# Kernel optimization log

Hardware: AMD Instinct MI355X
Metric: run time of the kernel (lower is better)

Reference implementation:

```python
import jax, jax.numpy as jnp
import numpy as np

GAMMA = 0.99
RHO_THRESHOLD = 1.0
C_THRESHOLD = 1.0
BASELINE_LOSS_SCALING = 0.5
ENT_COEFF = 0.01
PPO_CLIP = 0.2


def setup_inputs() -> dict:
    key = jax.random.key(0)
    ks = jax.random.split(key, 7)
    T, B, A = 512, 8192, 2
    return {
        "prob": jax.random.uniform(ks[0], (T, B, A), dtype=jnp.float32),
        "action_prob": jax.random.uniform(ks[1], (T, B, A), dtype=jnp.float32),
        "v": jax.random.normal(ks[2], (T, B), dtype=jnp.float32),
        "next_v": jax.random.normal(ks[3], (T, B), dtype=jnp.float32),
        "reward": jax.random.normal(ks[4], (T, B), dtype=jnp.float32),
        "action": jax.random.randint(ks[5], (T, B), 0, 2, dtype=jnp.int32),
        "done": jax.random.randint(ks[6], (T, B), 0, 2, dtype=jnp.int32),
    }


def _log_prob(p, a):
    # torch.distributions.Categorical normalizes unnormalized probs
    logp = jnp.log(p) - jnp.log(p.sum(-1, keepdims=True))  # [T,B,A]
    return jnp.take_along_axis(logp, a[..., None].astype(jnp.int32), axis=-1)[..., 0]


def reference(prob, action_prob, v, next_v, reward, action, done):
    done_f = done.astype(v.dtype)  # [T,B]
    logp = _log_prob(prob, action)
    logp_act = _log_prob(action_prob, action)
    ratio = jnp.exp(logp - logp_act)  # [T,B]

    clipped_rho = jnp.minimum(ratio, RHO_THRESHOLD)
    clipped_c = jnp.minimum(ratio, C_THRESHOLD)
    deltas = clipped_rho * (reward + (1.0 - done_f) * GAMMA * next_v - v)

    # V-trace backward recurrence over time (dim 0), vectorized over batch
    def step(next_vtrace, xs):
        v_t, d_t, c_t, rho_t, r_t, nv_t, dn_t = xs
        vt = v_t + d_t + GAMMA * c_t * (next_vtrace - nv_t) * (1.0 - dn_t)
        adv = rho_t * (r_t + GAMMA * next_vtrace * (1.0 - dn_t) - v_t)
        return vt, (vt, adv)

    _, (vtrace, adv) = jax.lax.scan(
        step, next_v[-1],
        (v, deltas, clipped_c, clipped_rho, reward, next_v, done_f),
        reverse=True)

    vtrace = jax.lax.stop_gradient(vtrace)  # .detach() in original
    adv = jax.lax.stop_gradient(adv)

    critic_loss = BASELINE_LOSS_SCALING * jnp.mean((v - vtrace) ** 2)
    surr1 = ratio * adv
    surr2 = jnp.clip(ratio, 1.0 - PPO_CLIP, 1.0 + PPO_CLIP) * adv
    actor_loss = -jnp.minimum(surr1, surr2).mean()

    # entropy is logged but NOT included in total_loss in the original
    total_loss = actor_loss + critic_loss
    return total_loss
```

## Files before the change

kernel.cpp:

```cpp
#include <hip/hip_runtime.h>

#define T_DIM 512
#define B_DIM 8192
#define GB 16
#define NC 32
#define LC 16
#define GAMMA 0.99f

__launch_bounds__(512, 4)
__global__ void vtrace_main(const float* __restrict__ prob,
                            const float* __restrict__ aprob,
                            const float* __restrict__ v,
                            const float* __restrict__ nv,
                            const float* __restrict__ rw,
                            const int* __restrict__ act,
                            const int* __restrict__ dnn,
                            float* __restrict__ partials) {
    __shared__ float Sc[NC][GB];
    __shared__ float Mc[NC][GB];
    __shared__ float Cin[NC][GB];
    __shared__ float red[16];

    const int tid = threadIdx.x;
    const int bl  = tid & (GB - 1);
    const int c   = tid >> 4;
    const int b   = blockIdx.x * GB + bl;
    const int t0  = c * LC;

    float rat[LC], mm[LC], pp[LC], ss[LC];
    float S = 0.0f, M = 1.0f;

    const float2* __restrict__ prob2  = (const float2*)prob;
    const float2* __restrict__ aprob2 = (const float2*)aprob;

#pragma unroll
    for (int i = LC - 1; i >= 0; --i) {
        const size_t idx = (size_t)(t0 + i) * B_DIM + b;
        float2 pr = prob2[idx];
        float2 qr = aprob2[idx];
        float vv  = v[idx];
        float nvv = nv[idx];
        float rr  = rw[idx];
        int   a   = act[idx];
        int   d   = dnn[idx];

        float pa    = a ? pr.y : pr.x;
        float qa    = a ? qr.y : qr.x;
        float ratio = (pa * (qr.x + qr.y)) / ((pr.x + pr.y) * qa);
        float rho   = fminf(ratio, 1.0f);
        float m     = d ? 0.0f : GAMMA * rho;
        float p     = rho * (rr - vv);
        (void)nvv;

        rat[i] = ratio; mm[i] = m; pp[i] = p; ss[i] = vv + p;
        S = ss[i] + m * S;
        M = m * M;
    }

    Sc[c][bl] = S;
    Mc[c][bl] = M;
    __syncthreads();

    if (tid < GB) {
        float carry = nv[(size_t)(T_DIM - 1) * B_DIM + blockIdx.x * GB + tid];
        for (int cc = NC - 1; cc >= 0; --cc) {
            Cin[cc][tid] = carry;
            carry = Sc[cc][tid] + Mc[cc][tid] * carry;
        }
    }
    __syncthreads();

    float carry  = Cin[c][bl];
    float critic = 0.0f, msum = 0.0f;
#pragma unroll
    for (int i = LC - 1; i >= 0; --i) {
        float adv = pp[i] + mm[i] * carry;
        carry     = ss[i] + mm[i] * carry;
        critic += adv * adv;
        float r_ = rat[i];
        float rc = fminf(fmaxf(r_, 0.8f), 1.2f);
        msum += fminf(r_ * adv, rc * adv);
    }

#pragma unroll
    for (int off = 32; off > 0; off >>= 1) {
        critic += __shfl_down(critic, off, 64);
        msum   += __shfl_down(msum, off, 64);
    }
    const int wave = tid >> 6;
    if ((tid & 63) == 0) { red[wave] = critic; red[8 + wave] = msum; }
    __syncthreads();
    if (tid == 0) {
        float cs = 0.0f, ms = 0.0f;
#pragma unroll
        for (int w = 0; w < 8; ++w) { cs += red[w]; ms += red[8 + w]; }
        partials[blockIdx.x]       = cs;
        partials[512 + blockIdx.x] = ms;
    }
}

__global__ void vtrace_final(const float* __restrict__ partials,
                             float* __restrict__ out) {
    __shared__ float red[16];
    const int tid = threadIdx.x;
    float cs = partials[tid];
    float ms = partials[512 + tid];
#pragma unroll
    for (int off = 32; off > 0; off >>= 1) {
        cs += __shfl_down(cs, off, 64);
        ms += __shfl_down(ms, off, 64);
    }
    const int wave = tid >> 6;
    if ((tid & 63) == 0) { red[wave] = cs; red[8 + wave] = ms; }
    __syncthreads();
    if (tid == 0) {
        float c = 0.0f, m = 0.0f;
#pragma unroll
        for (int w = 0; w < 8; ++w) { c += red[w]; m += red[8 + w]; }
        const float invN = 1.0f / (float)((size_t)T_DIM * B_DIM);
        out[0] = 0.5f * c * invN - m * invN;
    }
}

extern "C" void kernel_launch(void* const* d_in, const int* in_sizes, int n_in,
                              void* d_out, int out_size, void* d_ws, size_t ws_size,
                              hipStream_t stream) {
    const float* prob  = (const float*)d_in[0];
    const float* aprob = (const float*)d_in[1];
    const float* v     = (const float*)d_in[2];
    const float* nv    = (const float*)d_in[3];
    const float* rw    = (const float*)d_in[4];
    const int*   act   = (const int*)d_in[5];
    const int*   dnn   = (const int*)d_in[6];
    float* partials = (float*)d_ws;
    float* out      = (float*)d_out;

    vtrace_main<<<B_DIM / GB, GB * NC, 0, stream>>>(prob, aprob, v, nv, rw,
                                                    act, dnn, partials);
    vtrace_final<<<1, 512, 0, stream>>>(partials, out);
}
```

Measured before the change: 166.7 us.

## Halve time chunk length, pack done flag into ratio sign, cut registers

```diff
diff --git a/kernel.cpp b/kernel.cpp
--- a/kernel.cpp
+++ b/kernel.cpp
@@ -3,11 +3,11 @@
 #define T_DIM 512
 #define B_DIM 8192
 #define GB 16
-#define NC 32
-#define LC 16
+#define NC 64
+#define LC 8
 #define GAMMA 0.99f
 
-__launch_bounds__(512, 4)
+__launch_bounds__(1024, 8)
 __global__ void vtrace_main(const float* __restrict__ prob,
                             const float* __restrict__ aprob,
                             const float* __restrict__ v,
@@ -19,7 +19,7 @@
     __shared__ float Sc[NC][GB];
     __shared__ float Mc[NC][GB];
     __shared__ float Cin[NC][GB];
-    __shared__ float red[16];
+    __shared__ float red[32];
 
     const int tid = threadIdx.x;
     const int bl  = tid & (GB - 1);
@@ -27,7 +27,7 @@
     const int b   = blockIdx.x * GB + bl;
     const int t0  = c * LC;
 
-    float rat[LC], mm[LC], pp[LC], ss[LC];
+    float rs[LC], pp[LC], vv[LC];
     float S = 0.0f, M = 1.0f;
 
     const float2* __restrict__ prob2  = (const float2*)prob;
@@ -38,8 +38,7 @@
         const size_t idx = (size_t)(t0 + i) * B_DIM + b;
         float2 pr = prob2[idx];
         float2 qr = aprob2[idx];
-        float vv  = v[idx];
-        float nvv = nv[idx];
+        float vvi = v[idx];
         float rr  = rw[idx];
         int   a   = act[idx];
         int   d   = dnn[idx];
@@ -49,11 +48,12 @@
         float ratio = (pa * (qr.x + qr.y)) / ((pr.x + pr.y) * qa);
         float rho   = fminf(ratio, 1.0f);
         float m     = d ? 0.0f : GAMMA * rho;
-        float p     = rho * (rr - vv);
-        (void)nvv;
+        float p     = rho * (rr - vvi);
 
-        rat[i] = ratio; mm[i] = m; pp[i] = p; ss[i] = vv + p;
-        S = ss[i] + m * S;
+        rs[i] = __uint_as_float(__float_as_uint(ratio) | ((unsigned)d << 31));
+        pp[i] = p;
+        vv[i] = vvi;
+        S = (vvi + p) + m * S;
         M = m * M;
     }
 
@@ -63,9 +63,10 @@
 
     if (tid < GB) {
         float carry = nv[(size_t)(T_DIM - 1) * B_DIM + blockIdx.x * GB + tid];
+#pragma unroll 8
         for (int cc = NC - 1; cc >= 0; --cc) {
             Cin[cc][tid] = carry;
-            carry = Sc[cc][tid] + Mc[cc][tid] * carry;
+            carry = fmaf(Mc[cc][tid], carry, Sc[cc][tid]);
         }
     }
     __syncthreads();
@@ -74,12 +75,15 @@
     float critic = 0.0f, msum = 0.0f;
 #pragma unroll
     for (int i = LC - 1; i >= 0; --i) {
-        float adv = pp[i] + mm[i] * carry;
-        carry     = ss[i] + mm[i] * carry;
-        critic += adv * adv;
-        float r_ = rat[i];
-        float rc = fminf(fmaxf(r_, 0.8f), 1.2f);
-        msum += fminf(r_ * adv, rc * adv);
+        const unsigned u = __float_as_uint(rs[i]);
+        const float r   = __uint_as_float(u & 0x7fffffffu);
+        const float m   = ((int)u < 0) ? 0.0f : GAMMA * fminf(r, 1.0f);
+        const float adv = pp[i] + m * carry;
+        carry = vv[i] + adv;
+        critic = fmaf(adv, adv, critic);
+        const float lo = fminf(r, 1.2f);
+        const float hi = fmaxf(r, 0.8f);
+        msum += (adv >= 0.0f) ? lo * adv : hi * adv;
     }
 
 #pragma unroll
@@ -88,12 +92,12 @@
         msum   += __shfl_down(msum, off, 64);
     }
     const int wave = tid >> 6;
-    if ((tid & 63) == 0) { red[wave] = critic; red[8 + wave] = msum; }
+    if ((tid & 63) == 0) { red[wave] = critic; red[16 + wave] = msum; }
     __syncthreads();
     if (tid == 0) {
         float cs = 0.0f, ms = 0.0f;
 #pragma unroll
-        for (int w = 0; w < 8; ++w) { cs += red[w]; ms += red[8 + w]; }
+        for (int w = 0; w < 16; ++w) { cs += red[w]; ms += red[16 + w]; }
         partials[blockIdx.x]       = cs;
         partials[512 + blockIdx.x] = ms;
     }
```

Result: slower. 170.2 us (+2.1%).
